# Kernel tuning notes

Measured on AMD Instinct MI355X. Metric: run time of the kernel, lower is better.

## Reference

```python
import jax, jax.numpy as jnp
import numpy as np

D = 6       # stalk_dimension
RANK = 2    # low-rank factor


def setup_inputs() -> dict:
    key = jax.random.key(0)
    k = jax.random.split(key, 8)
    N, E, NNZ, F = 100000, 20000, 1000000, 64
    x = jax.random.normal(k[0], (N * D, F), dtype=jnp.float32)
    e = jax.random.normal(k[1], (E * D, F), dtype=jnp.float32)
    W = jax.random.normal(k[2], (2 * F, 2 * D * RANK + D), dtype=jnp.float32) * 0.05
    b = jnp.zeros((2 * D * RANK + D,), dtype=jnp.float32)
    row = jax.random.randint(k[3], (NNZ,), 0, N, dtype=jnp.int64)
    col = jax.random.randint(k[4], (NNZ,), 0, E, dtype=jnp.int64)
    hyperedge_index = jnp.stack([row, col], axis=0)
    node_types = jax.random.randint(k[5], (N,), 0, 4, dtype=jnp.int64)
    hyperedge_types = jax.random.randint(k[6], (E,), 0, 6, dtype=jnp.int64)
    return {"x": x, "e": e, "W": W, "b": b,
            "hyperedge_index": hyperedge_index,
            "node_types": node_types, "hyperedge_types": hyperedge_types}


def reference(x, e, W, b, hyperedge_index, node_types, hyperedge_types):
    d, r = D, RANK
    num_nodes = x.shape[0] // d
    num_edges = e.shape[0] // d
    # mean over stalk copies -> [N, F], [E, F]
    x = x.reshape(num_nodes, d, x.shape[-1]).mean(axis=1)
    e = e.reshape(num_edges, d, e.shape[-1]).mean(axis=1)
    row, col = hyperedge_index[0], hyperedge_index[1]
    # var1 he-features: identity; local_concat sheaf predictor
    h = jnp.concatenate([x[row], e[col]], axis=-1)          # [nnz, 2F]
    h_sheaf = jax.nn.sigmoid(h @ W + b)                     # [nnz, 2*d*r + d]
    A = h_sheaf[:, : d * r].reshape(-1, d, r)
    B = h_sheaf[:, d * r: 2 * d * r].reshape(-1, d, r)
    C = h_sheaf[:, 2 * d * r:]                              # [nnz, d]
    maps = jnp.einsum('nir,njr->nij', A, B)                 # A @ B^T
    maps = maps + C[:, :, None] * jnp.eye(d, dtype=maps.dtype)  # diag_embed(C)
    h_attrs = maps.reshape(-1)                              # [nnz*d*d]
    # sparse COO index construction
    dr = jnp.arange(d, dtype=row.dtype)
    off_nodes = jnp.repeat(dr, d)                           # repeat_interleave
    off_edges = jnp.tile(dr, d)                             # repeat
    idx0 = (d * row[:, None] + off_nodes[None, :]).reshape(-1)
    idx1 = (d * col[:, None] + off_edges[None, :]).reshape(-1)
    h_sheaf_index = jnp.stack([idx0, idx1], axis=0)         # [2, nnz*d*d]
    return (h_sheaf_index, h_attrs)
```

## Files before the change

### kernel.cpp

```cpp
#include <hip/hip_runtime.h>
#include <hip/hip_bf16.h>

#define DD 6
#define FF 64
#define NS 30
#define TS16 32
#define UPB 32

typedef float fx4 __attribute__((ext_vector_type(4)));

__device__ __forceinline__ float fast_sigmoid(float v) {
    return __builtin_amdgcn_rcpf(1.0f + __expf(-v));
}
__device__ __forceinline__ void nt_store4(float* p, float a, float b, float c, float d) {
    fx4 v = {a, b, c, d};
    __builtin_nontemporal_store(v, (fx4*)p);
}


__device__ __forceinline__ void precompute_body(
    const float* __restrict__ x, const float* __restrict__ e,
    const float* __restrict__ W, const float* __restrict__ bias,
    __hip_bfloat16* __restrict__ xW, __hip_bfloat16* __restrict__ eW,
    int N, int E, int nbN, int blk)
{
    __shared__ float means[UPB][68];
    bool isNode = blk < nbN;
    int ucount  = isNode ? N : E;
    int ubase   = (isNode ? blk : (blk - nbN)) * UPB;
    const float* src = isNode ? x : e;
    const float* Wp  = W + (isNode ? 0 : FF * NS);
    __hip_bfloat16* dst = isNode ? xW : eW;

    int tid = threadIdx.x, wid = tid >> 6, lane = tid & 63;

    #pragma unroll
    for (int i = 0; i < 8; ++i) {
        int s = wid * 8 + i;
        int u = ubase + s;
        float m = 0.f;
        if (u < ucount) {
            const float* p = src + (size_t)u * (DD * FF) + lane;
            #pragma unroll
            for (int d = 0; d < DD; ++d) m += p[d * FF];
        }
        means[s][lane] = m * (1.0f / 6.0f);
    }
    __syncthreads();

    int j30 = lane & 31;
    bool jval = j30 < NS;
    int j = jval ? j30 : 0;
    float wreg[FF];
    #pragma unroll
    for (int f = 0; f < FF; ++f) wreg[f] = Wp[f * NS + j];
    float bj = isNode ? bias[j] : 0.f;

    #pragma unroll
    for (int t = 0; t < 4; ++t) {
        int sl = wid * 8 + 2 * t + (lane >> 5);
        int u  = ubase + sl;
        const fx4* mp4 = (const fx4*)(&means[sl][0]);
        float o = bj;
        #pragma unroll
        for (int q = 0; q < 16; ++q) {
            fx4 m4 = mp4[q];
            o = fmaf(m4.x, wreg[4 * q + 0], o);
            o = fmaf(m4.y, wreg[4 * q + 1], o);
            o = fmaf(m4.z, wreg[4 * q + 2], o);
            o = fmaf(m4.w, wreg[4 * q + 3], o);
        }
        if (jval && u < ucount)
            dst[(size_t)u * TS16 + j30] = __float2bfloat16(o);
    }
}

__device__ __forceinline__ void idx_body(
    const int* __restrict__ rows, const int* __restrict__ cols,
    float* __restrict__ out_idx0, float* __restrict__ out_idx1,
    int tot, int ib)
{
    int g = (ib * 256 + (int)threadIdx.x) * 4;
    if (g >= tot) return;
    float v0[4], v1[4];
    #pragma unroll
    for (int i = 0; i < 4; ++i) {
        int gg = g + i;
        int l  = gg / 36;
        int m  = gg - l * 36;
        int m6 = m / 6;
        v0[i] = (float)(6 * rows[l] + m6);
        v1[i] = (float)(6 * cols[l] + (m - m6 * 6));
    }
    nt_store4(out_idx0 + g, v0[0], v0[1], v0[2], v0[3]);
    nt_store4(out_idx1 + g, v1[0], v1[1], v1[2], v1[3]);
}

__global__ __launch_bounds__(256) void pre_idx_kernel(
    const float* __restrict__ x, const float* __restrict__ e,
    const float* __restrict__ W, const float* __restrict__ bias,
    __hip_bfloat16* __restrict__ xW, __hip_bfloat16* __restrict__ eW,
    const int* __restrict__ rows, const int* __restrict__ cols,
    float* __restrict__ out_idx0, float* __restrict__ out_idx1,
    int N, int E, int nbN, int nbPre, int nnz)
{
    if ((int)blockIdx.x < nbPre) {
        precompute_body(x, e, W, bias, xW, eW, N, E, nbN, (int)blockIdx.x);
    } else {
        idx_body(rows, cols, out_idx0, out_idx1, nnz * 36, (int)blockIdx.x - nbPre);
    }
}

__global__ __launch_bounds__(256) void sheaf_kernel(
    const int* __restrict__ rows, const int* __restrict__ cols,
    const __hip_bfloat16* __restrict__ xW, const __hip_bfloat16* __restrict__ eW,
    float* __restrict__ out_attr, int nnz)
{
    __shared__ float mlds[4][32 * 37];
    int tid = threadIdx.x, wid = tid >> 6, lane = tid & 63;
    int bb  = blockIdx.x * 256;
    int k   = bb + tid;
    bool act = k < nnz;
    float mp[36];
    if (act) {
        int r = rows[k];
        int c = cols[k];
        const uint4* xp = (const uint4*)(xW + (size_t)r * TS16);
        const uint4* ep = (const uint4*)(eW + (size_t)c * TS16);
        uint4 xa0 = xp[0], xa1 = xp[1], xa2 = xp[2], xa3 = xp[3];
        uint4 ea0 = ep[0], ea1 = ep[1], ea2 = ep[2], ea3 = ep[3];
        uint wx[16] = {xa0.x, xa0.y, xa0.z, xa0.w, xa1.x, xa1.y, xa1.z, xa1.w,
                       xa2.x, xa2.y, xa2.z, xa2.w, xa3.x, xa3.y, xa3.z, xa3.w};
        uint we[16] = {ea0.x, ea0.y, ea0.z, ea0.w, ea1.x, ea1.y, ea1.z, ea1.w,
                       ea2.x, ea2.y, ea2.z, ea2.w, ea3.x, ea3.y, ea3.z, ea3.w};
        float s[NS];
        #pragma unroll
        for (int j2 = 0; j2 < NS; ++j2) {
            uint ux = (j2 & 1) ? (wx[j2 >> 1] & 0xffff0000u) : (wx[j2 >> 1] << 16);
            uint ue = (j2 & 1) ? (we[j2 >> 1] & 0xffff0000u) : (we[j2 >> 1] << 16);
            s[j2] = fast_sigmoid(__uint_as_float(ux) + __uint_as_float(ue));
        }
        #pragma unroll
        for (int i = 0; i < DD; ++i) {
            float a0 = s[i * 2], a1 = s[i * 2 + 1];
            #pragma unroll
            for (int jj = 0; jj < DD; ++jj) {
                float v = fmaf(a0, s[12 + jj * 2], a1 * s[13 + jj * 2]);
                if (i == jj) v += s[24 + i];
                mp[i * 6 + jj] = v;
            }
        }
    }
    float* wl = mlds[wid];
    int wbase = bb + wid * 64;
    #pragma unroll
    for (int h = 0; h < 2; ++h) {
        if (h) __syncthreads();
        if (act && (lane >> 5) == h) {
            float* ml = wl + (lane & 31) * 37;
            #pragma unroll
            for (int m = 0; m < 36; ++m) ml[m] = mp[m];
        }
        __syncthreads();
        int b2  = wbase + h * 32;
        int cnt = nnz - b2; if (cnt > 32) cnt = 32;
        if (cnt > 0) {
            int tot = cnt * 36;
            float* gp = out_attr + (size_t)b2 * 36;
            for (int g = lane * 4; g < tot; g += 256) {
                int l = g / 36;
                int m = g - l * 36;
                const float* mlp = wl + l * 37 + m;
                nt_store4(gp + g, mlp[0], mlp[1], mlp[2], mlp[3]);
            }
        }
    }
}

__global__ __launch_bounds__(256) void idx_kernel(
    const int* __restrict__ rows, const int* __restrict__ cols,
    float* __restrict__ out_idx0, float* __restrict__ out_idx1, int tot)
{
    idx_body(rows, cols, out_idx0, out_idx1, tot, (int)blockIdx.x);
}

extern "C" void kernel_launch(void* const* d_in, const int* in_sizes, int n_in,
                              void* d_out, int out_size, void* d_ws, size_t ws_size,
                              hipStream_t stream)
{
    const float* x = (const float*)d_in[0];
    const float* e = (const float*)d_in[1];
    const float* W = (const float*)d_in[2];
    const float* b = (const float*)d_in[3];
    const int* hidx = (const int*)d_in[4];

    int N   = in_sizes[0] / (DD * FF);
    int E   = in_sizes[1] / (DD * FF);
    int nnz = in_sizes[4] / 2;
    const int* rows = hidx;
    const int* cols = hidx + nnz;

    float* out = (float*)d_out;
    size_t M = (size_t)nnz * 36;
    float* out_idx0 = out;
    float* out_idx1 = out + M;
    float* out_attr = out + 2 * M;

    size_t tableBytes = ((size_t)N + (size_t)E) * TS16 * sizeof(__hip_bfloat16);
    bool haveWs = (ws_size >= tableBytes);
    __hip_bfloat16* xW = haveWs ? (__hip_bfloat16*)d_ws
                                : (__hip_bfloat16*)out_idx0;
    __hip_bfloat16* eW = xW + (size_t)N * TS16;

    int nbN = (N + UPB - 1) / UPB;
    int nbE = (E + UPB - 1) / UPB;
    int nbPre = nbN + nbE;
    int tot = nnz * 36;
    int iBlocks = (tot / 4 + 255) / 256;
    int sBlocks = (nnz + 255) / 256;

    if (haveWs) {
        pre_idx_kernel<<<nbPre + iBlocks, 256, 0, stream>>>(
            x, e, W, b, xW, eW, rows, cols, out_idx0, out_idx1,
            N, E, nbN, nbPre, nnz);
        sheaf_kernel<<<sBlocks, 256, 0, stream>>>(rows, cols, xW, eW, out_attr, nnz);
    } else {
        pre_idx_kernel<<<nbPre, 256, 0, stream>>>(
            x, e, W, b, xW, eW, rows, cols, out_idx0, out_idx1,
            N, E, nbN, nbPre, nnz);
        sheaf_kernel<<<sBlocks, 256, 0, stream>>>(rows, cols, xW, eW, out_attr, nnz);
        idx_kernel<<<iBlocks, 256, 0, stream>>>(rows, cols, out_idx0, out_idx1, tot);
    }
}
```

Baseline: 123.1 us.

## Interleave index-stream blocks with sheaf blocks and drop block barriers

The index-output writes move out of the precompute launch and into the sheaf launch. Sheaf blocks are spread evenly among index blocks so the gather-heavy map computation overlaps with the pure-store index streams. The index writer now handles one output array per block, 8 elements per thread, and loads a single index per 4-wide group. The sheaf staging drops `__syncthreads` in favour of compiler barriers, since each wave only touches its own LDS slice. This relies on lockstep LDS ordering within a wavefront.

New measurement: 274.9 us. +123.4%, slower.

```diff
diff --git a/kernel.cpp b/kernel.cpp
--- a/kernel.cpp
+++ b/kernel.cpp
@@ -16,7 +16,6 @@
     fx4 v = {a, b, c, d};
     __builtin_nontemporal_store(v, (fx4*)p);
 }
-
 
 __device__ __forceinline__ void precompute_body(
     const float* __restrict__ x, const float* __restrict__ e,
@@ -75,50 +74,39 @@
     }
 }
 
-__device__ __forceinline__ void idx_body(
-    const int* __restrict__ rows, const int* __restrict__ cols,
-    float* __restrict__ out_idx0, float* __restrict__ out_idx1,
-    int tot, int ib)
-{
-    int g = (ib * 256 + (int)threadIdx.x) * 4;
+__device__ __forceinline__ void idx_stream_body(
+    const int* __restrict__ ind, float* __restrict__ outp,
+    int tot, int ib, bool isDiv)
+{
+    int g = (ib * 256 + (int)threadIdx.x) * 8;
     if (g >= tot) return;
-    float v0[4], v1[4];
-    #pragma unroll
-    for (int i = 0; i < 4; ++i) {
-        int gg = g + i;
-        int l  = gg / 36;
-        int m  = gg - l * 36;
-        int m6 = m / 6;
-        v0[i] = (float)(6 * rows[l] + m6);
-        v1[i] = (float)(6 * cols[l] + (m - m6 * 6));
-    }
-    nt_store4(out_idx0 + g, v0[0], v0[1], v0[2], v0[3]);
-    nt_store4(out_idx1 + g, v1[0], v1[1], v1[2], v1[3]);
-}
-
-__global__ __launch_bounds__(256) void pre_idx_kernel(
-    const float* __restrict__ x, const float* __restrict__ e,
-    const float* __restrict__ W, const float* __restrict__ bias,
-    __hip_bfloat16* __restrict__ xW, __hip_bfloat16* __restrict__ eW,
-    const int* __restrict__ rows, const int* __restrict__ cols,
-    float* __restrict__ out_idx0, float* __restrict__ out_idx1,
-    int N, int E, int nbN, int nbPre, int nnz)
-{
-    if ((int)blockIdx.x < nbPre) {
-        precompute_body(x, e, W, bias, xW, eW, N, E, nbN, (int)blockIdx.x);
-    } else {
-        idx_body(rows, cols, out_idx0, out_idx1, nnz * 36, (int)blockIdx.x - nbPre);
-    }
-}
-
-__global__ __launch_bounds__(256) void sheaf_kernel(
+    #pragma unroll
+    for (int h = 0; h < 2; ++h) {
+        int gg = g + h * 4;
+        if (gg < tot) {
+            int l = gg / 36;
+            int m = gg - l * 36;
+            float base = (float)(6 * ind[l]);
+            float v[4];
+            #pragma unroll
+            for (int i = 0; i < 4; ++i) {
+                int mm = m + i;
+                int q6 = mm / 6;
+                v[i] = base + (float)(isDiv ? q6 : (mm - q6 * 6));
+            }
+            nt_store4(outp + gg, v[0], v[1], v[2], v[3]);
+        }
+    }
+}
+
+__device__ __forceinline__ void sheaf_body(
     const int* __restrict__ rows, const int* __restrict__ cols,
     const __hip_bfloat16* __restrict__ xW, const __hip_bfloat16* __restrict__ eW,
-    float* __restrict__ out_attr, int nnz)
+    float* __restrict__ out_attr, int nnz, int blk)
 {
     __shared__ float mlds[4][32 * 37];
     int tid = threadIdx.x, wid = tid >> 6, lane = tid & 63;
-    int bb  = blockIdx.x * 256;
+    int bb  = blk * 256;
     int k   = bb + tid;
     bool act = k < nnz;
     float mp[36];
@@ -155,13 +143,12 @@
     int wbase = bb + wid * 64;
     #pragma unroll
     for (int h = 0; h < 2; ++h) {
-        if (h) __syncthreads();
         if (act && (lane >> 5) == h) {
             float* ml = wl + (lane & 31) * 37;
             #pragma unroll
             for (int m = 0; m < 36; ++m) ml[m] = mp[m];
         }
-        __syncthreads();
+        asm volatile("" ::: "memory");
         int b2  = wbase + h * 32;
         int cnt = nnz - b2; if (cnt > 32) cnt = 32;
         if (cnt > 0) {
@@ -174,14 +161,48 @@
                 nt_store4(gp + g, mlp[0], mlp[1], mlp[2], mlp[3]);
             }
         }
-    }
-}
-
-__global__ __launch_bounds__(256) void idx_kernel(
+        asm volatile("" ::: "memory");
+    }
+}
+
+__global__ __launch_bounds__(256) void precompute_kernel(
+    const float* __restrict__ x, const float* __restrict__ e,
+    const float* __restrict__ W, const float* __restrict__ bias,
+    __hip_bfloat16* __restrict__ xW, __hip_bfloat16* __restrict__ eW,
+    int N, int E, int nbN)
+{
+    precompute_body(x, e, W, bias, xW, eW, N, E, nbN, (int)blockIdx.x);
+}
+
+__global__ __launch_bounds__(256) void sheaf_idx_kernel(
     const int* __restrict__ rows, const int* __restrict__ cols,
-    float* __restrict__ out_idx0, float* __restrict__ out_idx1, int tot)
-{
-    idx_body(rows, cols, out_idx0, out_idx1, tot, (int)blockIdx.x);
+    const __hip_bfloat16* __restrict__ xW, const __hip_bfloat16* __restrict__ eW,
+    float* __restrict__ out_attr,
+    float* __restrict__ out_idx0, float* __restrict__ out_idx1,
+    int nnz, int nS, int P, int nI0)
+{
+    int i = (int)blockIdx.x;
+    int q = i / P, rem = i - q * P;
+    if (rem == 0 && q < nS) {
+        sheaf_body(rows, cols, xW, eW, out_attr, nnz, q);
+        return;
+    }
+    int nsee = q + (rem ? 1 : 0); if (nsee > nS) nsee = nS;
+    int j = i - nsee;
+    int tot = nnz * 36;
+    if (j < nI0) idx_stream_body(rows, out_idx0, tot, j, true);
+    else         idx_stream_body(cols, out_idx1, tot, j - nI0, false);
+}
+
+__global__ __launch_bounds__(256) void idx0_kernel(
+    const int* __restrict__ rows, float* __restrict__ out_idx0, int tot)
+{
+    idx_stream_body(rows, out_idx0, tot, (int)blockIdx.x, true);
+}
+__global__ __launch_bounds__(256) void idx1_kernel(
+    const int* __restrict__ cols, float* __restrict__ out_idx1, int tot)
+{
+    idx_stream_body(cols, out_idx1, tot, (int)blockIdx.x, false);
 }
 
 extern "C" void kernel_launch(void* const* d_in, const int* in_sizes, int n_in,
@@ -216,19 +237,20 @@
     int nbE = (E + UPB - 1) / UPB;
     int nbPre = nbN + nbE;
     int tot = nnz * 36;
-    int iBlocks = (tot / 4 + 255) / 256;
-    int sBlocks = (nnz + 255) / 256;
+    int nI0 = (tot + 2047) / 2048;
+    int nS  = (nnz + 255) / 256;
+
+    precompute_kernel<<<nbPre, 256, 0, stream>>>(x, e, W, b, xW, eW, N, E, nbN);
 
     if (haveWs) {
-        pre_idx_kernel<<<nbPre + iBlocks, 256, 0, stream>>>(
-            x, e, W, b, xW, eW, rows, cols, out_idx0, out_idx1,
-            N, E, nbN, nbPre, nnz);
-        sheaf_kernel<<<sBlocks, 256, 0, stream>>>(rows, cols, xW, eW, out_attr, nnz);
+        int grid = nS + 2 * nI0;
+        int P = grid / nS; if (P < 1) P = 1;
+        sheaf_idx_kernel<<<grid, 256, 0, stream>>>(
+            rows, cols, xW, eW, out_attr, out_idx0, out_idx1, nnz, nS, P, nI0);
     } else {
-        pre_idx_kernel<<<nbPre, 256, 0, stream>>>(
-            x, e, W, b, xW, eW, rows, cols, out_idx0, out_idx1,
-            N, E, nbN, nbPre, nnz);
-        sheaf_kernel<<<sBlocks, 256, 0, stream>>>(rows, cols, xW, eW, out_attr, nnz);
-        idx_kernel<<<iBlocks, 256, 0, stream>>>(rows, cols, out_idx0, out_idx1, tot);
-    }
-}
+        sheaf_idx_kernel<<<nS, 256, 0, stream>>>(
+            rows, cols, xW, eW, out_attr, out_idx0, out_idx1, nnz, nS, 1, 0);
+        idx0_kernel<<<nI0, 256, 0, stream>>>(rows, out_idx0, tot);
+        idx1_kernel<<<nI0, 256, 0, stream>>>(cols, out_idx1, tot);
+    }
+}
```
